# Kernel optimization log

Measured on AMD Instinct MI355X. Metric: run time of the kernel, lower is better.

Reference implementation:

```python
import jax, jax.numpy as jnp
import numpy as np

B = 32
N_PER = 4096
N = B * N_PER
E = 2_097_152
D_IN = 32
D_OUT = 32
NUM_G_RELS = 14
NUM_ATTN_RELS = 10


def setup_inputs() -> dict:
    key = jax.random.key(0)
    ks = jax.random.split(key, 12)
    feat = jax.random.normal(ks[0], (N, D_IN), jnp.float32)
    src = jax.random.randint(ks[1], (E,), 0, N)
    dst = jax.random.randint(ks[2], (E,), 0, N)
    etype = jax.random.randint(ks[3], (E,), 0, NUM_ATTN_RELS)
    norm = jax.random.uniform(ks[4], (E,), jnp.float32)
    index1 = jax.random.randint(ks[5], (N,), 0, 2)  # path-node mask
    # first NUM_G_RELS nodes of each subgraph carry distinct relation slots -> unique scatter indices
    index2 = jnp.tile((jnp.arange(N_PER) < NUM_G_RELS).astype(jnp.int32), B)
    f2 = jnp.tile(jnp.arange(N_PER) % NUM_G_RELS, B).astype(jnp.int32)
    tar_rel = jnp.tile((jnp.arange(N_PER) == 0).astype(jnp.int32), B)  # one target node per graph
    s = 0.1
    W_w = jax.random.normal(ks[6], (D_IN, D_OUT), jnp.float32) * s
    b_w = jnp.zeros((D_OUT,), jnp.float32)
    W2 = jax.random.normal(ks[7], (3 * D_OUT, D_OUT), jnp.float32) * s
    b2 = jnp.zeros((D_OUT,), jnp.float32)
    attn_rel_emb = jax.random.normal(ks[8], (NUM_ATTN_RELS, D_OUT), jnp.float32) * s
    self_loop_w = jax.random.normal(ks[9], (D_IN, D_OUT), jnp.float32) * s
    W_line = jax.random.normal(ks[10], (D_OUT, D_OUT), jnp.float32) * s
    b_line = jnp.zeros((D_OUT,), jnp.float32)
    zero_path = jax.random.normal(ks[11], (1, D_OUT), jnp.float32) * s
    return {"feat": feat, "norm": norm, "W_w": W_w, "b_w": b_w, "W2": W2, "b2": b2,
            "attn_rel_emb": attn_rel_emb, "self_loop_w": self_loop_w, "W_line": W_line,
            "b_line": b_line, "zero_path": zero_path, "src": src, "dst": dst, "etype": etype,
            "index1": index1, "index2": index2, "f2": f2, "tar_rel": tar_rel,
            "n_per": N_PER, "num_g_rels": NUM_G_RELS}


def reference(feat, norm, W_w, b_w, W2, b2, attn_rel_emb, self_loop_w, W_line, b_line,
              zero_path, src, dst, etype, index1, index2, f2, tar_rel, n_per, num_g_rels):
    n_nodes, _ = feat.shape
    D = W_w.shape[1]
    # --- edge-wise relation-gated MLP (msg_func) ---
    et = attn_rel_emb[etype]                       # [E, D]
    w1 = feat[src] @ W_w + b_w                     # [E, D]
    cat = jnp.concatenate([et + w1, et - w1, et * w1], axis=1)  # [E, 3D]
    msg = (cat @ W2 + b2) * norm[:, None]          # [E, D] (edge weight w == 1)
    # --- SumAggregator: sum of msgs (alpha = ones) + self-loop term ---
    h = jax.ops.segment_sum(msg, dst, num_segments=n_nodes) + feat @ self_loop_w
    nf = jax.nn.relu(h @ W_line + b_line)          # cg_node_feats [N, D]
    # --- per-subgraph relation scatter + path attention (vectorized over batch) ---
    Bn = n_nodes // n_per
    nf_b = nf.reshape(Bn, n_per, D)
    mask2 = index2.reshape(Bn, n_per) != 0
    f2b = f2.reshape(Bn, n_per) + 1                # index_offset = 1
    write_idx = jnp.where(mask2, f2b, num_g_rels + 1)  # route masked rows to dump slot

    def scatter_one(idx, feats):
        buf = jnp.zeros((num_g_rels + 2, D), nf.dtype).at[idx].set(feats)
        return buf[:num_g_rels + 1]

    batch_rel_emds = jax.vmap(scatter_one)(write_idx, nf_b)  # [B, num_g_rels+1, D]
    tar1 = (tar_rel.reshape(Bn, n_per) == 1).astype(nf.dtype)
    target_rel_emd = jnp.einsum('bn,bnd->bd', tar1, nf_b)    # [B, D] (one-hot select)
    p1 = index1.reshape(Bn, n_per) == 1
    scores = jnp.where(p1, jnp.einsum('bnd,bd->bn', nf_b, target_rel_emd), -1e30)
    alpha = jax.nn.softmax(scores, axis=1)                   # segmented softmax over path nodes
    agg = jnp.einsum('bn,bnd->bd', alpha, nf_b)
    path_agg_emd = jnp.where(p1.any(axis=1)[:, None], agg, zero_path)  # [B, D]
    return batch_rel_emds, target_rel_emd, path_agg_emd
```

## Files before the change

kernel.cpp:

```cpp
#include <hip/hip_runtime.h>


#define N_PER_C 4096
#define NGR 14
#define NAR 10
#define EPB 256
#define NZB 68
#define KSP 8

typedef unsigned short u16;
typedef unsigned int u32;
typedef _Float16 hv2 __attribute__((ext_vector_type(2)));
union U32H2 { u32 u; hv2 h; };

__device__ __forceinline__ float b2f(u16 u) {
    union { u32 i; float f; } x; x.i = ((u32)u) << 16; return x.f;
}
__device__ __forceinline__ u16 f2bf(float f) {
    union { float f; u32 i; } x; x.f = f;
    u32 r = x.i + 0x7fff + ((x.i >> 16) & 1);
    return (u16)(r >> 16);
}
__device__ __forceinline__ float LD(const void* p, size_t i, int isf32) {
    return isf32 ? ((const float*)p)[i] : b2f(((const u16*)p)[i]);
}
__device__ __forceinline__ void ST_OUT(void* p, size_t i, float v, int isf32) {
    if (isf32) ((float*)p)[i] = v;
    else ((u16*)p)[i] = f2bf(v);
}
__device__ __forceinline__ u32 pkh(float a, float b) {
    U32H2 c; c.h = (hv2){(_Float16)a, (_Float16)b}; return c.u;
}
__device__ __forceinline__ hv2 ash2(u32 w) { U32H2 c; c.u = w; return c.h; }

__device__ __forceinline__ void pk_atomic_add_f16(u32* addr, u32 val) {
#if __has_builtin(__builtin_amdgcn_global_atomic_fadd_v2f16)
    U32H2 c; c.u = val;
    __builtin_amdgcn_global_atomic_fadd_v2f16((hv2*)addr, c.h);
#else
    u32 old = *addr, assumed;
    do {
        assumed = old;
        U32H2 a, v, r; a.u = assumed; v.u = val;
        r.h = a.h + v.h;
        old = atomicCAS(addr, assumed, r.u);
    } while (old != assumed);
#endif
}

__device__ __forceinline__ int probe_flag(const u32* featw) {
    int cnt = 0;
#pragma unroll
    for (int i = 0; i < 256; i += 64) {
        u32 w = featw[i + (threadIdx.x & 63)];
        u32 lo = w & 0xffffu;
        u32 e = (lo >> 7) & 0xffu;
        cnt += ((e >= 100 && e <= 140) || lo == 0) ? 1 : 0;
    }
    unsigned long long m = __ballot(cnt >= 3);
    return (__popcll(m) < 32) ? 1 : 0;
}

__global__ __launch_bounds__(256) void k_prep(
        const u32* __restrict__ featw,
        const void* W_w, const void* b_w, const void* W2, const void* b2v,
        const void* attn, const void* slw, const void* W_line, const void* b_line,
        u32* __restrict__ outw, int out_size,
        float* Wwf, float* bwf, float* Af, float* slwf, float* Wlf, float* blf,
        u32* Cf2, u32* at2, u32* cb2, int* flag) {
    int t = threadIdx.x;
    int b = blockIdx.x;
    int isf32 = probe_flag(featw);
    if (b < NZB) {
        int words = isf32 ? out_size : out_size / 2;
        for (int i = b * 256 + t; i < words; i += NZB * 256) outw[i] = 0;
        return;
    }
    if (t == 0) flag[0] = isf32;
    for (int i = t; i < 1024; i += 256) {
        int k = i >> 5, c = i & 31;
        Wwf[i]  = LD(W_w, i, isf32);
        slwf[i] = LD(slw, i, isf32);
        Wlf[i]  = LD(W_line, i, isf32);
        Af[i]   = LD(W2, k * 32 + c, isf32) - LD(W2, (32 + k) * 32 + c, isf32);
    }
    for (int i = t; i < 512; i += 256) {
        int k = i >> 4, j2 = i & 15;
        Cf2[i] = pkh(LD(W2, (64 + k) * 32 + 2 * j2, isf32),
                     LD(W2, (64 + k) * 32 + 2 * j2 + 1, isf32));
    }
    for (int i = t; i < NAR * 16; i += 256) {
        int tt = i >> 4, j2 = i & 15;
        at2[i] = pkh(LD(attn, tt * 32 + 2 * j2, isf32),
                     LD(attn, tt * 32 + 2 * j2 + 1, isf32));
        float s0 = LD(b2v, 2 * j2, isf32), s1 = LD(b2v, 2 * j2 + 1, isf32);
        for (int k = 0; k < 32; ++k) {
            float a = LD(attn, tt * 32 + k, isf32);
            s0 += a * (LD(W2, k * 32 + 2 * j2, isf32) + LD(W2, (32 + k) * 32 + 2 * j2, isf32));
            s1 += a * (LD(W2, k * 32 + 2 * j2 + 1, isf32) + LD(W2, (32 + k) * 32 + 2 * j2 + 1, isf32));
        }
        cb2[i] = pkh(s0, s1);
    }
    if (t < 32) { bwf[t] = LD(b_w, t, isf32); blf[t] = LD(b_line, t, isf32); }
}

__global__ void k1_node(const void* __restrict__ feat, const float* __restrict__ Wwf,
                        const float* __restrict__ bwf, const float* __restrict__ slwf,
                        const float* __restrict__ Af, u32* __restrict__ gp,
                        u32* __restrict__ h, int N,
                        const int* __restrict__ flag) {
    int n = blockIdx.x * blockDim.x + threadIdx.x;
    if (n >= N) return;
    int isf32 = flag[0];
    float f[32];
    if (isf32) {
        const float4* fr = (const float4*)((const float*)feat + (size_t)n * 32);
#pragma unroll
        for (int q = 0; q < 8; ++q) {
            float4 v = fr[q];
            f[q * 4 + 0] = v.x; f[q * 4 + 1] = v.y; f[q * 4 + 2] = v.z; f[q * 4 + 3] = v.w;
        }
    } else {
        const uint4* fr = (const uint4*)((const u16*)feat + (size_t)n * 32);
#pragma unroll
        for (int q = 0; q < 4; ++q) {
            uint4 v = fr[q];
            u32 ww[4] = {v.x, v.y, v.z, v.w};
#pragma unroll
            for (int r = 0; r < 4; ++r) {
                f[q * 8 + 2 * r]     = b2f((u16)(ww[r] & 0xffff));
                f[q * 8 + 2 * r + 1] = b2f((u16)(ww[r] >> 16));
            }
        }
    }
    float g[32], hh[32];
#pragma unroll
    for (int j = 0; j < 32; ++j) { g[j] = bwf[j]; hh[j] = 0.f; }
#pragma unroll
    for (int k = 0; k < 32; ++k) {
        float fk = f[k];
#pragma unroll
        for (int j = 0; j < 32; ++j) {
            g[j]  += fk * Wwf[k * 32 + j];
            hh[j] += fk * slwf[k * 32 + j];
        }
    }
    float p[32];
#pragma unroll
    for (int j = 0; j < 32; ++j) p[j] = 0.f;
#pragma unroll
    for (int k = 0; k < 32; ++k) {
        float gk = g[k];
#pragma unroll
        for (int j = 0; j < 32; ++j) p[j] += gk * Af[k * 32 + j];
    }
    u32* go = gp + (size_t)n * 32;
#pragma unroll
    for (int q = 0; q < 16; ++q) go[q]      = pkh(g[2 * q], g[2 * q + 1]);
#pragma unroll
    for (int q = 0; q < 16; ++q) go[16 + q] = pkh(p[2 * q], p[2 * q + 1]);
    u32* ho = h + (size_t)n * 16;
#pragma unroll
    for (int q = 0; q < 16; ++q) ho[q] = pkh(hh[2 * q], hh[2 * q + 1]);
}

__global__ __launch_bounds__(256) void k2_edge(const int* __restrict__ src,
                        const int* __restrict__ dst,
                        const int* __restrict__ et, const void* __restrict__ norm,
                        const u32* __restrict__ gp, const u32* __restrict__ cb2,
                        const u32* __restrict__ at2, const u32* __restrict__ Cp,
                        u32* __restrict__ h, int E,
                        const int* __restrict__ flag) {
    __shared__ u32 pk_s[EPB][17];
    __shared__ int d_s[EPB];
    int tid = threadIdx.x;
    int e = blockIdx.x * EPB + tid;
    int isf32 = flag[0];

    if (e < E) {
        int s = src[e], d = dst[e], t = et[e];
        float nr = LD(norm, e, isf32);
        u32 gw[16], pw[16], aw[16], cw[16];
        {
            const uint4* gg = (const uint4*)(gp + (size_t)s * 32);
#pragma unroll
            for (int q = 0; q < 4; ++q) {
                uint4 v = gg[q];
                gw[q * 4] = v.x; gw[q * 4 + 1] = v.y; gw[q * 4 + 2] = v.z; gw[q * 4 + 3] = v.w;
            }
#pragma unroll
            for (int q = 0; q < 4; ++q) {
                uint4 v = gg[4 + q];
                pw[q * 4] = v.x; pw[q * 4 + 1] = v.y; pw[q * 4 + 2] = v.z; pw[q * 4 + 3] = v.w;
            }
            const uint4* a4 = (const uint4*)(at2 + t * 16);
            const uint4* c4 = (const uint4*)(cb2 + t * 16);
#pragma unroll
            for (int q = 0; q < 4; ++q) {
                uint4 v = a4[q];
                aw[q * 4] = v.x; aw[q * 4 + 1] = v.y; aw[q * 4 + 2] = v.z; aw[q * 4 + 3] = v.w;
                uint4 w = c4[q];
                cw[q * 4] = w.x; cw[q * 4 + 1] = w.y; cw[q * 4 + 2] = w.z; cw[q * 4 + 3] = w.w;
            }
        }
        hv2 xg2[16], acc2[16];
#pragma unroll
        for (int q = 0; q < 16; ++q) {
            xg2[q]  = ash2(gw[q]) * ash2(aw[q]);
            acc2[q] = ash2(cw[q]) + ash2(pw[q]);
        }
#pragma unroll
        for (int k = 0; k < 32; ++k) {
            _Float16 xs = xg2[k >> 1][k & 1];
            hv2 xkk = {xs, xs};
#pragma unroll
            for (int j2 = 0; j2 < 16; ++j2)
                acc2[j2] += ash2(Cp[k * 16 + j2]) * xkk;
        }
        _Float16 nh = (_Float16)nr;
        hv2 nr2 = {nh, nh};
#pragma unroll
        for (int q = 0; q < 16; ++q) {
            U32H2 c; c.h = acc2[q] * nr2;
            pk_s[tid][q] = c.u;
        }
        d_s[tid] = d;
    } else {
        d_s[tid] = -1;
    }
    __syncthreads();

    int w  = tid & 15;
    int r0 = tid >> 4;
#pragma unroll
    for (int it = 0; it < 16; ++it) {
        int r = r0 + (it << 4);
        int d = d_s[r];
        if (d >= 0) pk_atomic_add_f16(h + (size_t)d * 16 + w, pk_s[r][w]);
    }
}

__global__ __launch_bounds__(256) void k34_fused(const u32* __restrict__ h,
        const float* __restrict__ Wlf, const float* __restrict__ blf,
        const int* __restrict__ index2, const int* __restrict__ f2,
        const int* __restrict__ index1,
        void* __restrict__ out, size_t off_tar,
        float* __restrict__ part_m, float* __restrict__ part_l,
        float* __restrict__ part_a, const int* __restrict__ flag) {
    int blk = blockIdx.x;
    int b = blk / KSP, c = blk % KSP;
    int tid = threadIdx.x;
    int isf32 = flag[0];
    __shared__ float tg[32];
    __shared__ float red_m[256], red_l[256];
    __shared__ float red_a[256][33];

    if (tid < 32) {
        const u32* h0 = h + (size_t)b * N_PER_C * 16;
        float o = blf[tid];
#pragma unroll
        for (int k = 0; k < 32; ++k) {
            hv2 x = ash2(h0[k >> 1]);
            o += (float)x[k & 1] * Wlf[k * 32 + tid];
        }
        o = fmaxf(o, 0.f);
        tg[tid] = o;
        if (c == 0) ST_OUT(out, off_tar + (size_t)b * 32 + tid, o, isf32);
    }
    __syncthreads();
    float tv[32];
#pragma unroll
    for (int j = 0; j < 32; ++j) tv[j] = tg[j];

    float m = -1e30f, l = 0.f, a[32];
#pragma unroll
    for (int j = 0; j < 32; ++j) a[j] = 0.f;

    const int R = N_PER_C / KSP;
    for (int rr = 0; rr < R / 256; ++rr) {
        int n = b * N_PER_C + c * R + rr * 256 + tid;
        float hr[32];
        const uint4* h4 = (const uint4*)(h + (size_t)n * 16);
#pragma unroll
        for (int q = 0; q < 4; ++q) {
            uint4 v = h4[q];
            u32 ww[4] = {v.x, v.y, v.z, v.w};
#pragma unroll
            for (int r2 = 0; r2 < 4; ++r2) {
                hv2 x = ash2(ww[r2]);
                hr[q * 8 + 2 * r2]     = (float)x[0];
                hr[q * 8 + 2 * r2 + 1] = (float)x[1];
            }
        }
        float o[32];
#pragma unroll
        for (int j = 0; j < 32; ++j) o[j] = blf[j];
#pragma unroll
        for (int k = 0; k < 32; ++k) {
            float hk = hr[k];
#pragma unroll
            for (int j = 0; j < 32; ++j) o[j] += hk * Wlf[k * 32 + j];
        }
#pragma unroll
        for (int j = 0; j < 32; ++j) o[j] = fmaxf(o[j], 0.f);
        if (index2[n] != 0) {
            int idx = f2[n] + 1;
            if (idx >= 0 && idx <= NGR) {
                size_t bse = ((size_t)(b * (NGR + 1) + idx)) * 32;
#pragma unroll
                for (int j = 0; j < 32; ++j) ST_OUT(out, bse + j, o[j], isf32);
            }
        }
        if (index1[n] == 1) {
            float dot = 0.f;
#pragma unroll
            for (int j = 0; j < 32; ++j) dot += o[j] * tv[j];
            if (dot > m) {
                float cc = __expf(m - dot);
                l *= cc;
#pragma unroll
                for (int j = 0; j < 32; ++j) a[j] *= cc;
                m = dot;
            }
            float w = __expf(dot - m);
            l += w;
#pragma unroll
            for (int j = 0; j < 32; ++j) a[j] += w * o[j];
        }
    }
    red_m[tid] = m; red_l[tid] = l;
#pragma unroll
    for (int j = 0; j < 32; ++j) red_a[tid][j] = a[j];
    __syncthreads();
    for (int s = 128; s >= 1; s >>= 1) {
        if (tid < s) {
            float m1 = red_m[tid], m2 = red_m[tid + s];
            float M = fmaxf(m1, m2);
            float c1 = __expf(m1 - M), c2 = __expf(m2 - M);
            red_l[tid] = red_l[tid] * c1 + red_l[tid + s] * c2;
#pragma unroll
            for (int j = 0; j < 32; ++j)
                red_a[tid][j] = red_a[tid][j] * c1 + red_a[tid + s][j] * c2;
            red_m[tid] = M;
        }
        __syncthreads();
    }
    if (tid == 0) { part_m[blk] = red_m[0]; part_l[blk] = red_l[0]; }
    if (tid < 32) part_a[(size_t)blk * 32 + tid] = red_a[0][tid];
}

__global__ __launch_bounds__(64) void k4b_merge(const float* __restrict__ part_m,
                                                const float* __restrict__ part_l,
                                                const float* __restrict__ part_a,
                                                const void* __restrict__ zero_path,
                                                void* __restrict__ out,
                                                size_t off_path,
                                                const int* __restrict__ flag) {
    int b = blockIdx.x;
    int j = threadIdx.x;
    int isf32 = flag[0];
    if (j >= 32) return;
    float M = -1e30f;
#pragma unroll
    for (int i = 0; i < KSP; ++i) M = fmaxf(M, part_m[b * KSP + i]);
    float L = 0.f, A = 0.f;
#pragma unroll
    for (int i = 0; i < KSP; ++i) {
        float c = __expf(part_m[b * KSP + i] - M);
        L += part_l[b * KSP + i] * c;
        A += part_a[(size_t)(b * KSP + i) * 32 + j] * c;
    }
    float o = (L > 0.f) ? (A / L) : LD(zero_path, j, isf32);
    ST_OUT(out, off_path + (size_t)b * 32 + j, o, isf32);
}

extern "C" void kernel_launch(void* const* d_in, const int* in_sizes, int n_in,
                              void* d_out, int out_size, void* d_ws, size_t ws_size,
                              hipStream_t stream) {
    const void* feat     = d_in[0];
    const void* norm     = d_in[1];
    const void* W_w      = d_in[2];
    const void* b_w      = d_in[3];
    const void* W2       = d_in[4];
    const void* b2v      = d_in[5];
    const void* attn     = d_in[6];
    const void* slw      = d_in[7];
    const void* W_line   = d_in[8];
    const void* b_line   = d_in[9];
    const void* zeroPath = d_in[10];
    const int* src       = (const int*)d_in[11];
    const int* dst       = (const int*)d_in[12];
    const int* etype     = (const int*)d_in[13];
    const int* index1    = (const int*)d_in[14];
    const int* index2    = (const int*)d_in[15];
    const int* f2        = (const int*)d_in[16];

    int N  = in_sizes[0] / 32;
    int E  = in_sizes[1];
    int Bn = N / N_PER_C;

    char* base  = (char*)d_ws;
    int* flag   = (int*)base;
    float* Wwf  = (float*)(base + 64);
    float* bwf  = Wwf + 1024;
    float* Af   = bwf + 32;
    float* slwf = Af + 1024;
    float* Wlf  = slwf + 1024;
    float* blf  = Wlf + 1024;
    u32*  Cf2   = (u32*)(blf + 32);
    u32*  at2   = Cf2 + 512;
    u32*  cb2   = at2 + NAR * 16;
    float* part_m = (float*)(cb2 + NAR * 16);
    float* part_l = part_m + (size_t)Bn * KSP;
    float* part_a = part_l + (size_t)Bn * KSP;
    u32*  h     = (u32*)(part_a + (size_t)Bn * KSP * 32);
    u32*  gp    = h + (size_t)N * 16;

    size_t off_tar  = (size_t)Bn * (NGR + 1) * 32;
    size_t off_path = off_tar + (size_t)Bn * 32;

    k_prep<<<NZB + 1, 256, 0, stream>>>((const u32*)feat,
                                        W_w, b_w, W2, b2v, attn, slw, W_line, b_line,
                                        (u32*)d_out, out_size,
                                        Wwf, bwf, Af, slwf, Wlf, blf,
                                        Cf2, at2, cb2, flag);
    k1_node<<<(N + 255) / 256, 256, 0, stream>>>(feat, Wwf, bwf, slwf, Af, gp, h, N,
                                                 flag);
    k2_edge<<<(E + EPB - 1) / EPB, 256, 0, stream>>>(src, dst, etype, norm, gp, cb2,
                                                     at2, Cf2, h, E, flag);
    k34_fused<<<Bn * KSP, 256, 0, stream>>>(h, Wlf, blf, index2, f2, index1,
                                            d_out, off_tar,
                                            part_m, part_l, part_a, flag);
    k4b_merge<<<Bn, 64, 0, stream>>>(part_m, part_l, part_a, zeroPath,
                                     d_out, off_path, flag);
}
```

Measured before the change: 304.8 us.

## Replace edge atomic scatter with dst-bucketed CSR gather and factored per-node matmul

Edge messages are no longer computed per edge and accumulated with packed f16 atomics. Instead, edges are counted by destination, bucketed into a CSR-like payload holding src, etype and norm, and gathered per destination node. The linear algebra is factored so each node sums norm*g, norm*g*attn and per-type norm weights, then applies the A/C matrices once per node instead of once per edge. This trades the per-edge 32x32 f16 matmul and the atomic contention for a counting pass, a scan/alloc pass and a scatter pass with integer atomics, plus per-node load imbalance from variable degree.

```diff
diff --git a/kernel.cpp b/kernel.cpp
--- a/kernel.cpp
+++ b/kernel.cpp
@@ -4,7 +4,6 @@
 #define N_PER_C 4096
 #define NGR 14
 #define NAR 10
-#define EPB 256
 #define NZB 68
 #define KSP 8
 
@@ -32,21 +31,6 @@
     U32H2 c; c.h = (hv2){(_Float16)a, (_Float16)b}; return c.u;
 }
 __device__ __forceinline__ hv2 ash2(u32 w) { U32H2 c; c.u = w; return c.h; }
-
-__device__ __forceinline__ void pk_atomic_add_f16(u32* addr, u32 val) {
-#if __has_builtin(__builtin_amdgcn_global_atomic_fadd_v2f16)
-    U32H2 c; c.u = val;
-    __builtin_amdgcn_global_atomic_fadd_v2f16((hv2*)addr, c.h);
-#else
-    u32 old = *addr, assumed;
-    do {
-        assumed = old;
-        U32H2 a, v, r; a.u = assumed; v.u = val;
-        r.h = a.h + v.h;
-        old = atomicCAS(addr, assumed, r.u);
-    } while (old != assumed);
-#endif
-}
 
 __device__ __forceinline__ int probe_flag(const u32* featw) {
     int cnt = 0;
@@ -67,177 +51,240 @@
         const void* attn, const void* slw, const void* W_line, const void* b_line,
         u32* __restrict__ outw, int out_size,
         float* Wwf, float* bwf, float* Af, float* slwf, float* Wlf, float* blf,
-        u32* Cf2, u32* at2, u32* cb2, int* flag) {
+        float* Cf, float* ctf, u32* at2, u32* cnt, u32* allocp, int N, int* flag) {
     int t = threadIdx.x;
     int b = blockIdx.x;
     int isf32 = probe_flag(featw);
     if (b < NZB) {
         int words = isf32 ? out_size : out_size / 2;
         for (int i = b * 256 + t; i < words; i += NZB * 256) outw[i] = 0;
+        for (int i = b * 256 + t; i < N; i += NZB * 256) cnt[i] = 0u;
         return;
     }
-    if (t == 0) flag[0] = isf32;
+    if (t == 0) { flag[0] = isf32; allocp[0] = 0u; }
     for (int i = t; i < 1024; i += 256) {
         int k = i >> 5, c = i & 31;
         Wwf[i]  = LD(W_w, i, isf32);
         slwf[i] = LD(slw, i, isf32);
         Wlf[i]  = LD(W_line, i, isf32);
         Af[i]   = LD(W2, k * 32 + c, isf32) - LD(W2, (32 + k) * 32 + c, isf32);
-    }
-    for (int i = t; i < 512; i += 256) {
-        int k = i >> 4, j2 = i & 15;
-        Cf2[i] = pkh(LD(W2, (64 + k) * 32 + 2 * j2, isf32),
-                     LD(W2, (64 + k) * 32 + 2 * j2 + 1, isf32));
+        Cf[i]   = LD(W2, (64 + k) * 32 + c, isf32);
     }
     for (int i = t; i < NAR * 16; i += 256) {
-        int tt = i >> 4, j2 = i & 15;
-        at2[i] = pkh(LD(attn, tt * 32 + 2 * j2, isf32),
-                     LD(attn, tt * 32 + 2 * j2 + 1, isf32));
-        float s0 = LD(b2v, 2 * j2, isf32), s1 = LD(b2v, 2 * j2 + 1, isf32);
+        int tt = i >> 4, q = i & 15;
+        at2[i] = pkh(LD(attn, tt * 32 + 2 * q, isf32),
+                     LD(attn, tt * 32 + 2 * q + 1, isf32));
+    }
+    for (int i = t; i < NAR * 32; i += 256) {
+        int tt = i >> 5, j = i & 31;
+        float s = LD(b2v, j, isf32);
         for (int k = 0; k < 32; ++k) {
             float a = LD(attn, tt * 32 + k, isf32);
-            s0 += a * (LD(W2, k * 32 + 2 * j2, isf32) + LD(W2, (32 + k) * 32 + 2 * j2, isf32));
-            s1 += a * (LD(W2, k * 32 + 2 * j2 + 1, isf32) + LD(W2, (32 + k) * 32 + 2 * j2 + 1, isf32));
-        }
-        cb2[i] = pkh(s0, s1);
+            s += a * (LD(W2, k * 32 + j, isf32) + LD(W2, (32 + k) * 32 + j, isf32));
+        }
+        ctf[i] = s;
     }
     if (t < 32) { bwf[t] = LD(b_w, t, isf32); blf[t] = LD(b_line, t, isf32); }
 }
 
 __global__ void k1_node(const void* __restrict__ feat, const float* __restrict__ Wwf,
                         const float* __restrict__ bwf, const float* __restrict__ slwf,
-                        const float* __restrict__ Af, u32* __restrict__ gp,
-                        u32* __restrict__ h, int N,
+                        u32* __restrict__ gbuf, u32* __restrict__ h, int N,
+                        const int* __restrict__ dst, u32* __restrict__ cnt, int E,
                         const int* __restrict__ flag) {
-    int n = blockIdx.x * blockDim.x + threadIdx.x;
+    int gid = blockIdx.x * blockDim.x + threadIdx.x;
+    int isf32 = flag[0];
+    if (gid < N) {
+        int n = gid;
+        float f[32];
+        if (isf32) {
+            const float4* fr = (const float4*)((const float*)feat + (size_t)n * 32);
+#pragma unroll
+            for (int q = 0; q < 8; ++q) {
+                float4 v = fr[q];
+                f[q * 4 + 0] = v.x; f[q * 4 + 1] = v.y; f[q * 4 + 2] = v.z; f[q * 4 + 3] = v.w;
+            }
+        } else {
+            const uint4* fr = (const uint4*)((const u16*)feat + (size_t)n * 32);
+#pragma unroll
+            for (int q = 0; q < 4; ++q) {
+                uint4 v = fr[q];
+                u32 ww[4] = {v.x, v.y, v.z, v.w};
+#pragma unroll
+                for (int r = 0; r < 4; ++r) {
+                    f[q * 8 + 2 * r]     = b2f((u16)(ww[r] & 0xffff));
+                    f[q * 8 + 2 * r + 1] = b2f((u16)(ww[r] >> 16));
+                }
+            }
+        }
+        float g[32], hh[32];
+#pragma unroll
+        for (int j = 0; j < 32; ++j) { g[j] = bwf[j]; hh[j] = 0.f; }
+#pragma unroll
+        for (int k = 0; k < 32; ++k) {
+            float fk = f[k];
+#pragma unroll
+            for (int j = 0; j < 32; ++j) {
+                g[j]  += fk * Wwf[k * 32 + j];
+                hh[j] += fk * slwf[k * 32 + j];
+            }
+        }
+        u32* go = gbuf + (size_t)n * 16;
+#pragma unroll
+        for (int q = 0; q < 16; ++q) go[q] = pkh(g[2 * q], g[2 * q + 1]);
+        u32* ho = h + (size_t)n * 16;
+#pragma unroll
+        for (int q = 0; q < 16; ++q) ho[q] = pkh(hh[2 * q], hh[2 * q + 1]);
+    }
+    int stride = gridDim.x * blockDim.x;
+    for (int e = gid; e < E; e += stride) atomicAdd(&cnt[dst[e]], 1u);
+}
+
+__global__ __launch_bounds__(256) void kC_alloc(const u32* __restrict__ cnt,
+                                                u32* __restrict__ cur,
+                                                u32* __restrict__ allocp, int N) {
+    __shared__ u32 red[256];
+    __shared__ u32 basesh;
+    int tid = threadIdx.x;
+    int i0 = (blockIdx.x * 256 + tid) * 4;
+    uint4 c = make_uint4(0u, 0u, 0u, 0u);
+    if (i0 + 3 < N) {
+        c = *(const uint4*)(cnt + i0);
+    } else if (i0 < N) {
+        c.x = cnt[i0];
+        if (i0 + 1 < N) c.y = cnt[i0 + 1];
+        if (i0 + 2 < N) c.z = cnt[i0 + 2];
+    }
+    u32 s = c.x + c.y + c.z + c.w;
+    red[tid] = s;
+    __syncthreads();
+    for (int off = 1; off < 256; off <<= 1) {
+        u32 v = (tid >= off) ? red[tid - off] : 0u;
+        __syncthreads();
+        red[tid] += v;
+        __syncthreads();
+    }
+    if (tid == 255) basesh = atomicAdd(allocp, red[255]);
+    __syncthreads();
+    u32 b0 = basesh + red[tid] - s;
+    if (i0 + 3 < N) {
+        *(uint4*)(cur + i0) = make_uint4(b0, b0 + c.x, b0 + c.x + c.y,
+                                         b0 + c.x + c.y + c.z);
+    } else if (i0 < N) {
+        cur[i0] = b0;
+        if (i0 + 1 < N) cur[i0 + 1] = b0 + c.x;
+        if (i0 + 2 < N) cur[i0 + 2] = b0 + c.x + c.y;
+    }
+}
+
+__global__ __launch_bounds__(256) void kD_scatter(const int* __restrict__ src,
+        const int* __restrict__ dst, const int* __restrict__ et,
+        const void* __restrict__ norm, u32* __restrict__ cur,
+        uint2* __restrict__ pay, int E, const int* __restrict__ flag) {
+    int e = blockIdx.x * 256 + threadIdx.x;
+    if (e >= E) return;
+    int isf32 = flag[0];
+    u32 se = (u32)src[e] | ((u32)et[e] << 27);
+    float nr = LD(norm, e, isf32);
+    u32 pos = atomicAdd(&cur[dst[e]], 1u);
+    pay[pos] = make_uint2(se, __float_as_uint(nr));
+}
+
+__global__ __launch_bounds__(256) void k2_gather(const u32* __restrict__ gbuf,
+        const uint2* __restrict__ pay, const u32* __restrict__ cnt,
+        const u32* __restrict__ cur, const float* __restrict__ Af,
+        const float* __restrict__ Cf, const float* __restrict__ ctf,
+        const u32* __restrict__ at2, u32* __restrict__ h, int N) {
+    __shared__ u32 atl[16 * NAR];
+    int tid = threadIdx.x;
+    if (tid < 16 * NAR) {
+        int t = tid >> 4, q = tid & 15;
+        atl[q * NAR + t] = at2[tid];
+    }
+    __syncthreads();
+    int n = blockIdx.x * 256 + tid;
     if (n >= N) return;
-    int isf32 = flag[0];
-    float f[32];
-    if (isf32) {
-        const float4* fr = (const float4*)((const float*)feat + (size_t)n * 32);
-#pragma unroll
-        for (int q = 0; q < 8; ++q) {
-            float4 v = fr[q];
-            f[q * 4 + 0] = v.x; f[q * 4 + 1] = v.y; f[q * 4 + 2] = v.z; f[q * 4 + 3] = v.w;
-        }
-    } else {
-        const uint4* fr = (const uint4*)((const u16*)feat + (size_t)n * 32);
-#pragma unroll
-        for (int q = 0; q < 4; ++q) {
-            uint4 v = fr[q];
-            u32 ww[4] = {v.x, v.y, v.z, v.w};
-#pragma unroll
-            for (int r = 0; r < 4; ++r) {
-                f[q * 8 + 2 * r]     = b2f((u16)(ww[r] & 0xffff));
-                f[q * 8 + 2 * r + 1] = b2f((u16)(ww[r] >> 16));
-            }
-        }
-    }
-    float g[32], hh[32];
-#pragma unroll
-    for (int j = 0; j < 32; ++j) { g[j] = bwf[j]; hh[j] = 0.f; }
+
+    float yg[32], x[32], nt[NAR];
+#pragma unroll
+    for (int j = 0; j < 32; ++j) { yg[j] = 0.f; x[j] = 0.f; }
+#pragma unroll
+    for (int t = 0; t < NAR; ++t) nt[t] = 0.f;
+
+    u32 e0 = cur[n];
+    u32 s0 = e0 - cnt[n];
+    for (u32 i = s0; i < e0; i += 2) {
+        uint2 p0 = pay[i];
+        uint2 p1 = (i + 1 < e0) ? pay[i + 1] : make_uint2(0u, 0u);
+        int sn0 = (int)(p0.x & 0x07FFFFFFu); int t0 = (int)(p0.x >> 27);
+        int sn1 = (int)(p1.x & 0x07FFFFFFu); int t1 = (int)(p1.x >> 27);
+        const uint4* g0 = (const uint4*)(gbuf + (size_t)sn0 * 16);
+        const uint4* g1 = (const uint4*)(gbuf + (size_t)sn1 * 16);
+        uint4 A0 = g0[0], B0 = g0[1], C0 = g0[2], D0 = g0[3];
+        uint4 A1 = g1[0], B1 = g1[1], C1 = g1[2], D1 = g1[3];
+        float nr0 = __uint_as_float(p0.y);
+        float nr1 = __uint_as_float(p1.y);
+        u32 w0[16] = {A0.x, A0.y, A0.z, A0.w, B0.x, B0.y, B0.z, B0.w,
+                      C0.x, C0.y, C0.z, C0.w, D0.x, D0.y, D0.z, D0.w};
+        u32 w1[16] = {A1.x, A1.y, A1.z, A1.w, B1.x, B1.y, B1.z, B1.w,
+                      C1.x, C1.y, C1.z, C1.w, D1.x, D1.y, D1.z, D1.w};
+#pragma unroll
+        for (int q = 0; q < 16; ++q) {
+            hv2 gv = ash2(w0[q]);
+            hv2 av = ash2(atl[q * NAR + t0]);
+            float ng0 = nr0 * (float)gv[0];
+            float ng1 = nr0 * (float)gv[1];
+            yg[2 * q]     += ng0;
+            yg[2 * q + 1] += ng1;
+            x[2 * q]      += ng0 * (float)av[0];
+            x[2 * q + 1]  += ng1 * (float)av[1];
+        }
+#pragma unroll
+        for (int q = 0; q < 16; ++q) {
+            hv2 gv = ash2(w1[q]);
+            hv2 av = ash2(atl[q * NAR + t1]);
+            float ng0 = nr1 * (float)gv[0];
+            float ng1 = nr1 * (float)gv[1];
+            yg[2 * q]     += ng0;
+            yg[2 * q + 1] += ng1;
+            x[2 * q]      += ng0 * (float)av[0];
+            x[2 * q + 1]  += ng1 * (float)av[1];
+        }
+#pragma unroll
+        for (int t = 0; t < NAR; ++t) {
+            nt[t] += (t0 == t) ? nr0 : 0.f;
+            nt[t] += (t1 == t) ? nr1 : 0.f;
+        }
+    }
+
+    float o[32];
+    const uint4* hr4 = (const uint4*)(h + (size_t)n * 16);
+#pragma unroll
+    for (int q4 = 0; q4 < 4; ++q4) {
+        uint4 v = hr4[q4];
+        u32 ww[4] = {v.x, v.y, v.z, v.w};
+#pragma unroll
+        for (int r = 0; r < 4; ++r) {
+            hv2 xh = ash2(ww[r]);
+            o[q4 * 8 + 2 * r]     = (float)xh[0];
+            o[q4 * 8 + 2 * r + 1] = (float)xh[1];
+        }
+    }
+#pragma unroll
+    for (int t = 0; t < NAR; ++t) {
+        float w = nt[t];
+#pragma unroll
+        for (int j = 0; j < 32; ++j) o[j] += w * ctf[t * 32 + j];
+    }
 #pragma unroll
     for (int k = 0; k < 32; ++k) {
-        float fk = f[k];
-#pragma unroll
-        for (int j = 0; j < 32; ++j) {
-            g[j]  += fk * Wwf[k * 32 + j];
-            hh[j] += fk * slwf[k * 32 + j];
-        }
-    }
-    float p[32];
-#pragma unroll
-    for (int j = 0; j < 32; ++j) p[j] = 0.f;
-#pragma unroll
-    for (int k = 0; k < 32; ++k) {
-        float gk = g[k];
-#pragma unroll
-        for (int j = 0; j < 32; ++j) p[j] += gk * Af[k * 32 + j];
-    }
-    u32* go = gp + (size_t)n * 32;
-#pragma unroll
-    for (int q = 0; q < 16; ++q) go[q]      = pkh(g[2 * q], g[2 * q + 1]);
-#pragma unroll
-    for (int q = 0; q < 16; ++q) go[16 + q] = pkh(p[2 * q], p[2 * q + 1]);
+        float a = yg[k], b = x[k];
+#pragma unroll
+        for (int j = 0; j < 32; ++j) o[j] += a * Af[k * 32 + j] + b * Cf[k * 32 + j];
+    }
     u32* ho = h + (size_t)n * 16;
 #pragma unroll
-    for (int q = 0; q < 16; ++q) ho[q] = pkh(hh[2 * q], hh[2 * q + 1]);
-}
-
-__global__ __launch_bounds__(256) void k2_edge(const int* __restrict__ src,
-                        const int* __restrict__ dst,
-                        const int* __restrict__ et, const void* __restrict__ norm,
-                        const u32* __restrict__ gp, const u32* __restrict__ cb2,
-                        const u32* __restrict__ at2, const u32* __restrict__ Cp,
-                        u32* __restrict__ h, int E,
-                        const int* __restrict__ flag) {
-    __shared__ u32 pk_s[EPB][17];
-    __shared__ int d_s[EPB];
-    int tid = threadIdx.x;
-    int e = blockIdx.x * EPB + tid;
-    int isf32 = flag[0];
-
-    if (e < E) {
-        int s = src[e], d = dst[e], t = et[e];
-        float nr = LD(norm, e, isf32);
-        u32 gw[16], pw[16], aw[16], cw[16];
-        {
-            const uint4* gg = (const uint4*)(gp + (size_t)s * 32);
-#pragma unroll
-            for (int q = 0; q < 4; ++q) {
-                uint4 v = gg[q];
-                gw[q * 4] = v.x; gw[q * 4 + 1] = v.y; gw[q * 4 + 2] = v.z; gw[q * 4 + 3] = v.w;
-            }
-#pragma unroll
-            for (int q = 0; q < 4; ++q) {
-                uint4 v = gg[4 + q];
-                pw[q * 4] = v.x; pw[q * 4 + 1] = v.y; pw[q * 4 + 2] = v.z; pw[q * 4 + 3] = v.w;
-            }
-            const uint4* a4 = (const uint4*)(at2 + t * 16);
-            const uint4* c4 = (const uint4*)(cb2 + t * 16);
-#pragma unroll
-            for (int q = 0; q < 4; ++q) {
-                uint4 v = a4[q];
-                aw[q * 4] = v.x; aw[q * 4 + 1] = v.y; aw[q * 4 + 2] = v.z; aw[q * 4 + 3] = v.w;
-                uint4 w = c4[q];
-                cw[q * 4] = w.x; cw[q * 4 + 1] = w.y; cw[q * 4 + 2] = w.z; cw[q * 4 + 3] = w.w;
-            }
-        }
-        hv2 xg2[16], acc2[16];
-#pragma unroll
-        for (int q = 0; q < 16; ++q) {
-            xg2[q]  = ash2(gw[q]) * ash2(aw[q]);
-            acc2[q] = ash2(cw[q]) + ash2(pw[q]);
-        }
-#pragma unroll
-        for (int k = 0; k < 32; ++k) {
-            _Float16 xs = xg2[k >> 1][k & 1];
-            hv2 xkk = {xs, xs};
-#pragma unroll
-            for (int j2 = 0; j2 < 16; ++j2)
-                acc2[j2] += ash2(Cp[k * 16 + j2]) * xkk;
-        }
-        _Float16 nh = (_Float16)nr;
-        hv2 nr2 = {nh, nh};
-#pragma unroll
-        for (int q = 0; q < 16; ++q) {
-            U32H2 c; c.h = acc2[q] * nr2;
-            pk_s[tid][q] = c.u;
-        }
-        d_s[tid] = d;
-    } else {
-        d_s[tid] = -1;
-    }
-    __syncthreads();
-
-    int w  = tid & 15;
-    int r0 = tid >> 4;
-#pragma unroll
-    for (int it = 0; it < 16; ++it) {
-        int r = r0 + (it << 4);
-        int d = d_s[r];
-        if (d >= 0) pk_atomic_add_f16(h + (size_t)d * 16 + w, pk_s[r][w]);
-    }
+    for (int q = 0; q < 16; ++q) ho[q] = pkh(o[2 * q], o[2 * q + 1]);
 }
 
 __global__ __launch_bounds__(256) void k34_fused(const u32* __restrict__ h,
@@ -407,14 +454,22 @@
     float* slwf = Af + 1024;
     float* Wlf  = slwf + 1024;
     float* blf  = Wlf + 1024;
-    u32*  Cf2   = (u32*)(blf + 32);
-    u32*  at2   = Cf2 + 512;
-    u32*  cb2   = at2 + NAR * 16;
-    float* part_m = (float*)(cb2 + NAR * 16);
+    float* Cf   = blf + 32;
+    float* ctf  = Cf + 1024;
+    u32*  at2   = (u32*)(ctf + NAR * 32);
+    float* part_m = (float*)(at2 + NAR * 16);
     float* part_l = part_m + (size_t)Bn * KSP;
     float* part_a = part_l + (size_t)Bn * KSP;
-    u32*  h     = (u32*)(part_a + (size_t)Bn * KSP * 32);
-    u32*  gp    = h + (size_t)N * 16;
+    char* pa = (char*)(part_a + (size_t)Bn * KSP * 32);
+    pa = (char*)(((size_t)pa + 255) & ~(size_t)255);
+    u32* allocp = (u32*)pa;
+    u32* cnt    = allocp + 64;
+    u32* cur    = cnt + N;
+    char* pb = (char*)(cur + N);
+    pb = (char*)(((size_t)pb + 255) & ~(size_t)255);
+    uint2* pay  = (uint2*)pb;
+    u32* gbuf   = (u32*)(pay + (size_t)E);
+    u32* h      = gbuf + (size_t)N * 16;
 
     size_t off_tar  = (size_t)Bn * (NGR + 1) * 32;
     size_t off_path = off_tar + (size_t)Bn * 32;
@@ -423,11 +478,14 @@
                                         W_w, b_w, W2, b2v, attn, slw, W_line, b_line,
                                         (u32*)d_out, out_size,
                                         Wwf, bwf, Af, slwf, Wlf, blf,
-                                        Cf2, at2, cb2, flag);
-    k1_node<<<(N + 255) / 256, 256, 0, stream>>>(feat, Wwf, bwf, slwf, Af, gp, h, N,
-                                                 flag);
-    k2_edge<<<(E + EPB - 1) / EPB, 256, 0, stream>>>(src, dst, etype, norm, gp, cb2,
-                                                     at2, Cf2, h, E, flag);
+                                        Cf, ctf, at2, cnt, allocp, N, flag);
+    k1_node<<<(N + 255) / 256, 256, 0, stream>>>(feat, Wwf, bwf, slwf, gbuf, h, N,
+                                                 dst, cnt, E, flag);
+    kC_alloc<<<(N + 1023) / 1024, 256, 0, stream>>>(cnt, cur, allocp, N);
+    kD_scatter<<<(E + 255) / 256, 256, 0, stream>>>(src, dst, etype, norm, cur,
+                                                    pay, E, flag);
+    k2_gather<<<(N + 255) / 256, 256, 0, stream>>>(gbuf, pay, cnt, cur,
+                                                   Af, Cf, ctf, at2, h, N);
     k34_fused<<<Bn * KSP, 256, 0, stream>>>(h, Wlf, blf, index2, f2, index1,
                                             d_out, off_tar,
                                             part_m, part_l, part_a, flag);
```

After: 461.0 us. +51.3%, slower.
